# Performance work log

Hardware: AMD Instinct MI355X
Metric: run time of the kernel (lower is better)

## Reference

```python
import jax, jax.numpy as jnp
import numpy as np

N_EDGES = 1024
STALK_D = 8
N_UNDIR = 16384  # -> 32768 directed pairs
EPS = 1e-4


def setup_inputs() -> dict:
    key = jax.random.key(0)
    n = N_EDGES
    rng = np.random.default_rng(0)
    a = rng.integers(0, n, size=80000)
    b = rng.integers(0, n, size=80000)
    m = a != b
    lo = np.minimum(a[m], b[m])
    hi = np.maximum(a[m], b[m])
    uniq = np.unique(lo * n + hi)
    rng.shuffle(uniq)
    uniq = uniq[:N_UNDIR]
    lo, hi = uniq // n, uniq % n
    directed = np.concatenate([np.stack([lo, hi], 1), np.stack([hi, lo], 1)], 0)
    edge_indices = jnp.asarray(directed, dtype=jnp.int32)  # (P,2), every pair has its reverse
    P = edge_indices.shape[0]
    k1, k2 = jax.random.split(key)
    restriction_matrices = jax.random.normal(k1, (P, STALK_D, STALK_D), dtype=jnp.float32)
    L1 = jax.random.normal(k2, (n, n), dtype=jnp.float32)
    return {"restriction_matrices": restriction_matrices, "edge_indices": edge_indices,
            "num_edges": n, "L1": L1}


def _edge_sheaf_laplacian(R, edge_indices, n, L1):
    d = R.shape[-1]
    P = R.shape[0]
    i = edge_indices[:, 0]
    j = edge_indices[:, 1]

    # Diagonal blocks: sum_p F_p^T F_p scattered by source edge i
    FtF = jnp.einsum('pki,pkj->pij', R, R)              # (P,d,d) = F^T F
    diag = jax.ops.segment_sum(FtF, i, num_segments=n)  # (n,d,d)

    # Reverse-pair lookup: find idx of (j,i) for each (i,j) via sorted key search
    keys = i.astype(jnp.int64) * n + j.astype(jnp.int64)
    order = jnp.argsort(keys)
    sk = keys[order]
    rev = j.astype(jnp.int64) * n + i.astype(jnp.int64)
    pos = jnp.clip(jnp.searchsorted(sk, rev), 0, P - 1)
    found = sk[pos] == rev
    ji_idx = order[pos]

    F_ji = R[ji_idx]                                    # (P,d,d)
    sgn = jnp.sign(L1[i, j])
    off = -sgn[:, None, None] * jnp.einsum('pki,pkj->pij', F_ji, R)  # -sign * F_ji^T @ F_ij
    off = jnp.where(found[:, None, None], off, jnp.zeros((), off.dtype))

    # Assemble block matrix LF as (n,d,n,d): off-diagonal set, diagonal add (i != j always)
    LF4 = jnp.zeros((n, d, n, d), dtype=R.dtype)
    LF4 = LF4.at[i, :, j, :].set(off)
    ar = jnp.arange(n)
    LF4 = LF4.at[ar, :, ar, :].add(diag)

    # Block-diagonal D^{-1/2} via batched eigh of symmetrized diagonal blocks
    D = (diag + jnp.swapaxes(diag, 1, 2)) * 0.5 + EPS * jnp.eye(d, dtype=R.dtype)
    w, V = jnp.linalg.eigh(D)
    w = jnp.clip(w, EPS)
    Dis = jnp.einsum('nij,nj,nkj->nik', V, 1.0 / jnp.sqrt(w), V)  # (n,d,d)

    # Delta = D^{-1/2} LF D^{-1/2}; D^{-1/2} is block-diagonal -> blockwise sandwich
    Delta4 = jnp.einsum('iab,ibjc,jcd->iajd', Dis, LF4, Dis)
    return Delta4.reshape(n * d, n * d)


def reference(restriction_matrices, edge_indices, num_edges, L1):
    return _edge_sheaf_laplacian(restriction_matrices, edge_indices, int(num_edges), L1)
```

## Files before the change

kernel.cpp:

```cpp
#include <hip/hip_runtime.h>
#include <cstddef>
#include <cstdint>


namespace {
constexpr int N = 1024;
constexpr int ND = 8192;
constexpr int MAXB = 96;
}

__global__ __launch_bounds__(256) void k_build(const float* __restrict__ R,
                                               const int* __restrict__ eidx, int P,
                                               int* __restrict__ cnt,
                                               int* __restrict__ rowlist,
                                               float* __restrict__ diag) {
  int gid = blockIdx.x * blockDim.x + threadIdx.x;
  int u = gid >> 6;
  if (u >= P) return;
  const int lane = gid & 63;
  const int a = lane >> 3, b = lane & 7;
  int2 e = ((const int2*)eidx)[u];
  float r = R[(size_t)u * 64 + lane];
  float acc = 0.f;
#pragma unroll
  for (int k = 0; k < 8; ++k)
    acc += __shfl(r, k * 8 + a, 64) * __shfl(r, k * 8 + b, 64);
  atomicAdd(&diag[e.x * 64 + lane], acc);
  if (lane == 0) {
    int slot = atomicAdd(&cnt[e.x], 1);
    if (slot < MAXB) rowlist[e.x * MAXB + slot] = u;
  }
}

__global__ __launch_bounds__(256) void k_invsqrt(const float* __restrict__ diag,
                                                 float* __restrict__ Dis) {
  const int tid = threadIdx.x;
  const int wid = tid >> 6, lane = tid & 63;
  const int a = lane >> 3, b = lane & 7;
  const int v = (blockIdx.x << 2) + wid;
  float dv = diag[v * 64 + lane];
  float A = dv + (a == b ? 1e-4f : 0.f);
  float sq = A * A;
#pragma unroll
  for (int off = 32; off; off >>= 1) sq += __shfl_xor(sq, off, 64);
  float fro = sqrtf(sq);
  float Y = A * (1.f / fro);
  float Z = (a == b) ? 1.f : 0.f;
  for (int it = 0; it < 14; ++it) {
    float T = 0.f;
#pragma unroll
    for (int k = 0; k < 8; ++k)
      T += __shfl(Z, a * 8 + k, 64) * __shfl(Y, k * 8 + b, 64);
    float G = ((a == b) ? 1.5f : 0.f) - 0.5f * T;
    float Yn = 0.f, Zn = 0.f;
#pragma unroll
    for (int k = 0; k < 8; ++k) {
      Yn += __shfl(Y, a * 8 + k, 64) * __shfl(G, k * 8 + b, 64);
      Zn += __shfl(G, a * 8 + k, 64) * __shfl(Z, k * 8 + b, 64);
    }
    Y = Yn;
    Z = Zn;
  }
  Dis[v * 64 + lane] = Z * (1.f / sqrtf(fro));
}

__global__ __launch_bounds__(256) void k_out(
    const float* __restrict__ R, const int* __restrict__ eidx,
    const float* __restrict__ L1, const int* __restrict__ cnt,
    const int* __restrict__ rowlist, const float* __restrict__ diag,
    const float* __restrict__ Dis, int P, float* __restrict__ out) {
  const int i = blockIdx.x;
  const int tid = threadIdx.x;
  const int wid = tid >> 6, lane = tid & 63;
  const int a = lane >> 3, b = lane & 7;
  __shared__ float Bc[MAXB + 1][64];
  __shared__ short map[N];
  __shared__ int sp[MAXB], srev[MAXB], sj[MAXB];
  __shared__ float ssgn[MAXB];

  for (int t = tid; t < N; t += 256) map[t] = -1;
  int c = cnt[i];
  if (c > MAXB) c = MAXB;
  const int halfP = P >> 1;

  if (tid < c) {
    int p = rowlist[i * MAXB + tid];
    int2 e = ((const int2*)eidx)[p];
    int rev = (p < halfP) ? p + halfP : p - halfP;
    int2 er = ((const int2*)eidx)[rev];
    bool ok = (er.x == e.y) && (er.y == i);
    float l1v = L1[i * N + e.y];
    float sgn = (l1v > 0.f ? 1.f : 0.f) - (l1v < 0.f ? 1.f : 0.f);
    sp[tid] = p;
    srev[tid] = rev;
    sj[tid] = e.y;
    ssgn[tid] = ok ? -sgn : 0.f;
    map[e.y] = (short)(tid + 1);
  }
  if (tid == 0) map[i] = 0;
  __syncthreads();

  const float di = Dis[i * 64 + lane];
  if (wid == 0) {
    float M = diag[i * 64 + lane];
    float T = 0.f;
#pragma unroll
    for (int k = 0; k < 8; ++k)
      T += __shfl(M, a * 8 + k, 64) * __shfl(di, k * 8 + b, 64);
    float o = 0.f;
#pragma unroll
    for (int k = 0; k < 8; ++k)
      o += __shfl(di, a * 8 + k, 64) * __shfl(T, k * 8 + b, 64);
    Bc[0][lane] = o;
  }
  for (int s = wid; s < c; s += 4) {
    float sgn = ssgn[s];
    float o = 0.f;
    if (sgn != 0.f) {
      float rp = R[(size_t)sp[s] * 64 + lane];
      float rr = R[(size_t)srev[s] * 64 + lane];
      float dj = Dis[sj[s] * 64 + lane];
      float m = 0.f;
#pragma unroll
      for (int k = 0; k < 8; ++k)
        m += __shfl(rr, k * 8 + a, 64) * __shfl(rp, k * 8 + b, 64);
      m *= sgn;
      float T = 0.f;
#pragma unroll
      for (int k = 0; k < 8; ++k)
        T += __shfl(m, a * 8 + k, 64) * __shfl(dj, k * 8 + b, 64);
#pragma unroll
      for (int k = 0; k < 8; ++k)
        o += __shfl(di, a * 8 + k, 64) * __shfl(T, k * 8 + b, 64);
    }
    Bc[s + 1][lane] = o;
  }
  __syncthreads();

#pragma unroll
  for (int rrow = 0; rrow < 8; ++rrow) {
    float4* orow = (float4*)(out + (size_t)(i * 8 + rrow) * ND);
#pragma unroll
    for (int kk = 0; kk < 8; ++kk) {
      int c4 = kk * 256 + tid;
      int jb = c4 >> 1, half = c4 & 1;
      int slot = map[jb];
      float4 v = {0.f, 0.f, 0.f, 0.f};
      if (slot >= 0) v = *(const float4*)(&Bc[slot][rrow * 8 + half * 4]);
      orow[c4] = v;
    }
  }
}

extern "C" void kernel_launch(void* const* d_in, const int* in_sizes, int n_in,
                              void* d_out, int out_size, void* d_ws, size_t ws_size,
                              hipStream_t stream) {
  const float* R = (const float*)d_in[0];
  const int* eidx = (const int*)d_in[1];
  const float* L1 = (const float*)d_in[3];
  float* out = (float*)d_out;
  int P = in_sizes[0] / 64;

  int* cnt = (int*)d_ws;
  float* diag = (float*)(cnt + N);
  int* rowlist = (int*)(diag + (size_t)N * 64);
  float* Dis = (float*)(rowlist + (size_t)N * MAXB);

  hipMemsetAsync(cnt, 0, N * sizeof(int) + (size_t)N * 64 * sizeof(float), stream);
  k_build<<<(P * 64) / 256, 256, 0, stream>>>(R, eidx, P, cnt, rowlist, diag);
  k_invsqrt<<<N / 4, 256, 0, stream>>>(diag, Dis);
  k_out<<<N, 256, 0, stream>>>(R, eidx, L1, cnt, rowlist, diag, Dis, P, out);
}
```

Baseline: 88.28 us.

## Fuse memset, build, invsqrt and output into one cooperative kernel

Replaces the memset plus three kernel launches with a single cooperative kernel that uses grid-wide syncs between the zeroing, scatter, inverse-sqrt and output phases, with a fallback to the old path if the cooperative launch fails. The aim is to remove launch gaps and inter-kernel overhead. It also hoists the map lookups out of the output store loop into registers. Grid syncs add their own cost and need all 1024 blocks to be co-resident, which the shared-memory use may prevent, and then the launch would fall back.

New measurement: 333.0 us. +277.3%, slower.

```diff
diff --git a/kernel.cpp b/kernel.cpp
--- a/kernel.cpp
+++ b/kernel.cpp
@@ -1,12 +1,164 @@
 #include <hip/hip_runtime.h>
+#include <hip/hip_cooperative_groups.h>
 #include <cstddef>
 #include <cstdint>
+
+namespace cg = cooperative_groups;
 
 
 namespace {
 constexpr int N = 1024;
 constexpr int ND = 8192;
 constexpr int MAXB = 96;
+constexpr int GRID = 1024;
+constexpr int TPB = 256;
+}
+
+__global__ __launch_bounds__(256) void fused(const float* __restrict__ R,
+                                             const int* __restrict__ eidx,
+                                             const float* __restrict__ L1, int P,
+                                             int* __restrict__ cnt,
+                                             int* __restrict__ rowlist,
+                                             float* __restrict__ diag,
+                                             float* __restrict__ Dis,
+                                             float* __restrict__ out) {
+  const int tid = threadIdx.x;
+  const int bid = blockIdx.x;
+  const int wid = tid >> 6, lane = tid & 63;
+  const int a = lane >> 3, b = lane & 7;
+  const int gw = (bid << 2) + wid;
+
+  {
+    int gtid = bid * TPB + tid;
+    if (gtid < N + N * 64) cnt[gtid] = 0;
+  }
+  cg::this_grid().sync();
+
+  for (int u = gw; u < P; u += GRID * 4) {
+    int2 e = ((const int2*)eidx)[u];
+    float r = R[(size_t)u * 64 + lane];
+    float acc = 0.f;
+#pragma unroll
+    for (int k = 0; k < 8; ++k)
+      acc += __shfl(r, k * 8 + a, 64) * __shfl(r, k * 8 + b, 64);
+    atomicAdd(&diag[e.x * 64 + lane], acc);
+    if (lane == 0) {
+      int slot = atomicAdd(&cnt[e.x], 1);
+      if (slot < MAXB) rowlist[e.x * MAXB + slot] = u;
+    }
+  }
+  cg::this_grid().sync();
+
+  if (gw < N) {
+    const int v = gw;
+    float dv = diag[v * 64 + lane];
+    float A = dv + (a == b ? 1e-4f : 0.f);
+    float sq = A * A;
+#pragma unroll
+    for (int off = 32; off; off >>= 1) sq += __shfl_xor(sq, off, 64);
+    float fro = sqrtf(sq);
+    float Y = A * (1.f / fro);
+    float Z = (a == b) ? 1.f : 0.f;
+    for (int it = 0; it < 14; ++it) {
+      float T = 0.f;
+#pragma unroll
+      for (int k = 0; k < 8; ++k)
+        T += __shfl(Z, a * 8 + k, 64) * __shfl(Y, k * 8 + b, 64);
+      float G = ((a == b) ? 1.5f : 0.f) - 0.5f * T;
+      float Yn = 0.f, Zn = 0.f;
+#pragma unroll
+      for (int k = 0; k < 8; ++k) {
+        Yn += __shfl(Y, a * 8 + k, 64) * __shfl(G, k * 8 + b, 64);
+        Zn += __shfl(G, a * 8 + k, 64) * __shfl(Z, k * 8 + b, 64);
+      }
+      Y = Yn;
+      Z = Zn;
+    }
+    Dis[v * 64 + lane] = Z * (1.f / sqrtf(fro));
+  }
+  cg::this_grid().sync();
+
+  const int i = bid;
+  __shared__ float Bc[MAXB + 1][64];
+  __shared__ short map[N];
+  __shared__ int sp[MAXB], srev[MAXB], sj[MAXB];
+  __shared__ float ssgn[MAXB];
+
+  for (int t = tid; t < N; t += TPB) map[t] = -1;
+  int c = cnt[i];
+  if (c > MAXB) c = MAXB;
+  const int halfP = P >> 1;
+  __syncthreads();
+
+  if (tid < c) {
+    int p = rowlist[i * MAXB + tid];
+    int2 e = ((const int2*)eidx)[p];
+    int rev = (p < halfP) ? p + halfP : p - halfP;
+    int2 er = ((const int2*)eidx)[rev];
+    bool ok = (er.x == e.y) && (er.y == i);
+    float l1v = L1[i * N + e.y];
+    float sgn = (l1v > 0.f ? 1.f : 0.f) - (l1v < 0.f ? 1.f : 0.f);
+    sp[tid] = p;
+    srev[tid] = rev;
+    sj[tid] = e.y;
+    ssgn[tid] = ok ? -sgn : 0.f;
+    map[e.y] = (short)(tid + 1);
+  }
+  if (tid == 0) map[i] = 0;
+  __syncthreads();
+
+  const float di = Dis[i * 64 + lane];
+  if (wid == 0) {
+    float M = diag[i * 64 + lane];
+    float T = 0.f;
+#pragma unroll
+    for (int k = 0; k < 8; ++k)
+      T += __shfl(M, a * 8 + k, 64) * __shfl(di, k * 8 + b, 64);
+    float o = 0.f;
+#pragma unroll
+    for (int k = 0; k < 8; ++k)
+      o += __shfl(di, a * 8 + k, 64) * __shfl(T, k * 8 + b, 64);
+    Bc[0][lane] = o;
+  }
+  for (int s = wid; s < c; s += 4) {
+    float sgn = ssgn[s];
+    float o = 0.f;
+    if (sgn != 0.f) {
+      float rp = R[(size_t)sp[s] * 64 + lane];
+      float rr = R[(size_t)srev[s] * 64 + lane];
+      float dj = Dis[sj[s] * 64 + lane];
+      float m = 0.f;
+#pragma unroll
+      for (int k = 0; k < 8; ++k)
+        m += __shfl(rr, k * 8 + a, 64) * __shfl(rp, k * 8 + b, 64);
+      m *= sgn;
+      float T = 0.f;
+#pragma unroll
+      for (int k = 0; k < 8; ++k)
+        T += __shfl(m, a * 8 + k, 64) * __shfl(dj, k * 8 + b, 64);
+#pragma unroll
+      for (int k = 0; k < 8; ++k)
+        o += __shfl(di, a * 8 + k, 64) * __shfl(T, k * 8 + b, 64);
+    }
+    Bc[s + 1][lane] = o;
+  }
+  __syncthreads();
+
+  short s8[8];
+#pragma unroll
+  for (int kk = 0; kk < 8; ++kk) s8[kk] = map[kk * 128 + (tid >> 1)];
+  const int half4 = (tid & 1) * 4;
+#pragma unroll
+  for (int rrow = 0; rrow < 8; ++rrow) {
+    float4* orow = (float4*)(out + (size_t)(i * 8 + rrow) * ND);
+#pragma unroll
+    for (int kk = 0; kk < 8; ++kk) {
+      int slot = s8[kk];
+      float4 v = {0.f, 0.f, 0.f, 0.f};
+      if (slot >= 0) v = *(const float4*)(&Bc[slot][rrow * 8 + half4]);
+      orow[kk * 256 + tid] = v;
+    }
+  }
 }
 
 __global__ __launch_bounds__(256) void k_build(const float* __restrict__ R,
@@ -82,6 +234,7 @@
   int c = cnt[i];
   if (c > MAXB) c = MAXB;
   const int halfP = P >> 1;
+  __syncthreads();
 
   if (tid < c) {
     int p = rowlist[i * MAXB + tid];
@@ -137,17 +290,19 @@
   }
   __syncthreads();
 
+  short s8[8];
+#pragma unroll
+  for (int kk = 0; kk < 8; ++kk) s8[kk] = map[kk * 128 + (tid >> 1)];
+  const int half4 = (tid & 1) * 4;
 #pragma unroll
   for (int rrow = 0; rrow < 8; ++rrow) {
     float4* orow = (float4*)(out + (size_t)(i * 8 + rrow) * ND);
 #pragma unroll
     for (int kk = 0; kk < 8; ++kk) {
-      int c4 = kk * 256 + tid;
-      int jb = c4 >> 1, half = c4 & 1;
-      int slot = map[jb];
+      int slot = s8[kk];
       float4 v = {0.f, 0.f, 0.f, 0.f};
-      if (slot >= 0) v = *(const float4*)(&Bc[slot][rrow * 8 + half * 4]);
-      orow[c4] = v;
+      if (slot >= 0) v = *(const float4*)(&Bc[slot][rrow * 8 + half4]);
+      orow[kk * 256 + tid] = v;
     }
   }
 }
@@ -166,6 +321,12 @@
   int* rowlist = (int*)(diag + (size_t)N * 64);
   float* Dis = (float*)(rowlist + (size_t)N * MAXB);
 
+  void* args[] = {(void*)&R,   (void*)&eidx,    (void*)&L1,  (void*)&P, (void*)&cnt,
+                  (void*)&rowlist, (void*)&diag, (void*)&Dis, (void*)&out};
+  hipError_t e = hipLaunchCooperativeKernel((const void*)fused, dim3(GRID), dim3(TPB),
+                                            args, 0, stream);
+  if (e == hipSuccess) return;
+
   hipMemsetAsync(cnt, 0, N * sizeof(int) + (size_t)N * 64 * sizeof(float), stream);
   k_build<<<(P * 64) / 256, 256, 0, stream>>>(R, eidx, P, cnt, rowlist, diag);
   k_invsqrt<<<N / 4, 256, 0, stream>>>(diag, Dis);
```
